# Kernel tuning notes

Hardware: AMD Instinct MI355X
Metric: run time of the kernel (lower is better)

## Reference

```python
import jax, jax.numpy as jnp
import numpy as np
import itertools

# ---- static configuration (matches init_kwargs) ----
LS = [0, 1, 2, 3]            # spherical harmonic degrees, parity (-1)^l
MUL = 128                    # channel multiplicity of hklm / output
N_EDGES = 16384
DIMS = [2 * l + 1 for l in LS]
Y_DIM = sum(DIMS)                        # 16
H_DIM = sum(d * MUL for d in DIMS)       # 2048
Y_OFF = np.cumsum([0] + DIMS).tolist()
H_OFF = np.cumsum([0] + [d * MUL for d in DIMS]).tolist()

# ---- real-basis O(3) Clebsch-Gordan coefficients (numpy, setup-time) ----
def _su2_generators(l):
    m = np.arange(-l, l + 1)
    Lz = np.diag(m).astype(np.complex128)
    vals = np.sqrt(l * (l + 1) - m[:-1] * (m[:-1] + 1))
    Lp = np.zeros((2 * l + 1, 2 * l + 1), np.complex128)
    Lp[np.arange(1, 2 * l + 1), np.arange(2 * l)] = vals
    Lm = Lp.T.copy()
    return (Lp + Lm) / 2.0, (Lp - Lm) / 2.0j, Lz

def _c2r(l):
    # unitary change of basis: complex SH -> real SH
    d = 2 * l + 1
    U = np.zeros((d, d), np.complex128)
    U[l, l] = 1.0
    s2 = 1.0 / np.sqrt(2.0)
    for m in range(1, l + 1):
        U[l + m, l + m] = (-1) ** m * s2
        U[l + m, l - m] = s2
        U[l - m, l + m] = -1j * (-1) ** m * s2
        U[l - m, l - m] = 1j * s2
    return U

def _real_generators(l):
    U = _c2r(l)
    return [np.real(-1j * (U @ L @ U.conj().T)) for L in _su2_generators(l)]

def _cg(l1, l2, l3):
    # invariant tensor = null space of the summed infinitesimal rotation action
    G1, G2, G3 = _real_generators(l1), _real_generators(l2), _real_generators(l3)
    d1, d2, d3 = 2 * l1 + 1, 2 * l2 + 1, 2 * l3 + 1
    I1, I2, I3 = np.eye(d1), np.eye(d2), np.eye(d3)
    rows = []
    for k in range(3):
        rows.append(np.kron(np.kron(G1[k], I2), I3)
                    + np.kron(np.kron(I1, G2[k]), I3)
                    + np.kron(np.kron(I1, I2), G3[k]))
    K = np.concatenate(rows, axis=0)
    _, s, Vt = np.linalg.svd(K)
    c = Vt[-1].reshape(d1, d2, d3)
    c = c / np.linalg.norm(c)
    c = c * np.sign(c.reshape(-1)[np.argmax(np.abs(c))])  # deterministic sign
    return c

PATHS = []
_CG_LIST = []
for (i1, l1), (i2, l2), (i3, l3) in itertools.product(enumerate(LS), enumerate(LS), enumerate(LS)):
    # triangle inequality + O3 parity selection rule ((-1)^l parities)
    if abs(l1 - l2) <= l3 <= l1 + l2 and (l1 + l2 + l3) % 2 == 0:
        PATHS.append((i1, i2, i3))
        _CG_LIST.append(_cg(l1, l2, l3))
N_PATHS = len(PATHS)                    # 23
W_DIM = N_PATHS * MUL                   # 2944
CG_OFF = np.cumsum([0] + [c.size for c in _CG_LIST]).tolist()
CGC_NP = np.concatenate([c.reshape(-1) for c in _CG_LIST]).astype(np.float32)


def setup_inputs() -> dict:
    key = jax.random.key(0)
    k1, k2, k3 = jax.random.split(key, 3)
    return {
        "Ylm": jax.random.normal(k1, (N_EDGES, Y_DIM), jnp.float32),
        "hklm": jax.random.normal(k2, (N_EDGES, H_DIM), jnp.float32),
        "weight": jax.random.normal(k3, (N_EDGES, W_DIM), jnp.float32),
        "CGC": jnp.asarray(CGC_NP),   # registered buffer in the torch module
    }


def reference(Ylm, hklm, weight, CGC):
    # segmented tensor product 'abcu,a,bu,cu' with per-path weight fused in:
    # out[n, c, u] += sum_{a,b} CG_p[a,b,c] * w_p[n,u] * Y[n,a] * h[n,b,u]
    N = Ylm.shape[0]
    out = jnp.zeros((N, H_DIM), Ylm.dtype)
    for p, (i1, i2, i3) in enumerate(PATHS):
        d1, d2, d3 = DIMS[i1], DIMS[i2], DIMS[i3]
        cg = CGC[CG_OFF[p]:CG_OFF[p + 1]].reshape(d1, d2, d3)
        y = Ylm[:, Y_OFF[i1]:Y_OFF[i1] + d1]
        h = hklm[:, H_OFF[i2]:H_OFF[i2] + d2 * MUL].reshape(N, d2, MUL)
        w = weight[:, p * MUL:(p + 1) * MUL]
        z = jnp.einsum('abc,na,nbu->ncu', cg, y, h) * w[:, None, :]
        out = out.at[:, H_OFF[i3]:H_OFF[i3] + d3 * MUL].add(z.reshape(N, d3 * MUL))
    return out
```

## Files before the change

kernel.cpp:

```cpp
#include <hip/hip_runtime.h>


#define BS 256
#define EPB 2
#define TPE 128
#define YD 16
#define HD 2048
#define WD 2944
#define NROW 99

typedef float f4 __attribute__((ext_vector_type(4)));

#define FOR_PATHS(X) \
  X(0, 0,0,0,    0,  0) \
  X(1, 0,1,1,    1,  1) \
  X(2, 0,2,2,   10,  4) \
  X(3, 0,3,3,   35,  9) \
  X(4, 1,0,1,   84, 16) \
  X(5, 1,1,0,   93, 19) \
  X(6, 1,1,2,  102, 20) \
  X(7, 1,2,1,  147, 25) \
  X(8, 1,2,3,  192, 28) \
  X(9, 1,3,2,  297, 35) \
  X(10,2,0,2,  402, 40) \
  X(11,2,1,1,  427, 45) \
  X(12,2,1,3,  472, 48) \
  X(13,2,2,0,  577, 55) \
  X(14,2,2,2,  602, 56) \
  X(15,2,3,1,  727, 61) \
  X(16,2,3,3,  832, 64) \
  X(17,3,0,3, 1077, 71) \
  X(18,3,1,2, 1126, 78) \
  X(19,3,2,1, 1231, 83) \
  X(20,3,2,3, 1336, 86) \
  X(21,3,3,0, 1581, 93) \
  X(22,3,3,2, 1630, 94)

__host__ __device__ constexpr int coff(int l) {
  return l == 0 ? 0 : (l == 1 ? 1 : (l == 2 ? 4 : 9));
}

__global__ __launch_bounds__(BS, 8) void etp_kernel(
    const float* __restrict__ Y, const float* __restrict__ H,
    const float* __restrict__ W, const float* __restrict__ CG,
    float* __restrict__ O) {
  const int g = threadIdx.x >> 7;
  const int u = threadIdx.x & 127;
  const size_t n = (size_t)blockIdx.x * EPB + g;

  __shared__ __align__(16) float Bsm[EPB][NROW * 8];
  __shared__ float ysm[EPB][YD];

  { const int t = threadIdx.x;
    if (t < EPB * YD) {
      const int e = t >> 4, c = t & 15;
      ysm[e][c] = Y[(size_t)(blockIdx.x * EPB + e) * YD + c];
    } }
  __syncthreads();

#define BUILD(P, L1, L2, L3, CGO, RO) { \
    constexpr int d1 = 2*(L1)+1, d2 = 2*(L2)+1, d3 = 2*(L3)+1; \
    if (u < d2 * d3) { \
      const int m3 = u / d2, m2 = u - m3 * d2; \
      float s = 0.f; \
      _Pragma("unroll") \
      for (int a = 0; a < d1; ++a) \
        s += CG[(CGO) + (a * d2 + m2) * d3 + m3] * ysm[g][coff(L1) + a]; \
      Bsm[g][((RO) + m3) * 8 + m2] = s; \
    } }
  FOR_PATHS(BUILD)
#undef BUILD
  __syncthreads();

  const float* __restrict__ Hn = H + n * HD + u;
  const float* __restrict__ Wn = W + n * WD + u;
  float* __restrict__ On = O + n * HD + u;

  float acc[YD];
#pragma unroll
  for (int c = 0; c < YD; ++c) acc[c] = 0.f;

#define DOP(P, L2, L3, RO) { \
    constexpr int d2 = 2*(L2)+1, d3 = 2*(L3)+1; \
    const float wv = Wn[(P) * TPE]; \
    _Pragma("unroll") \
    for (int m3 = 0; m3 < d3; ++m3) { \
      const f4* row = (const f4*)&Bsm[g][((RO) + m3) * 8]; \
      float br[8]; \
      *(f4*)&br[0] = row[0]; \
      if (d2 > 4) *(f4*)&br[4] = row[1]; \
      float s = 0.f; \
      _Pragma("unroll") \
      for (int m2 = 0; m2 < d2; ++m2) s += br[m2] * hh[m2]; \
      acc[coff(L3) + m3] += s * wv; \
    } }

  {
    float hh[1];
    hh[0] = Hn[(coff(0) + 0) * TPE];
    DOP(0, 0, 0, 0)  DOP(4, 0, 1, 16)  DOP(10, 0, 2, 40)  DOP(17, 0, 3, 71)
  }
  {
    float hh[3];
#pragma unroll
    for (int m = 0; m < 3; ++m) hh[m] = Hn[(coff(1) + m) * TPE];
    DOP(1, 1, 1, 1)  DOP(5, 1, 0, 19)  DOP(6, 1, 2, 20)
    DOP(11, 1, 1, 45)  DOP(12, 1, 3, 48)  DOP(18, 1, 2, 78)
  }
  {
    float hh[5];
#pragma unroll
    for (int m = 0; m < 5; ++m) hh[m] = Hn[(coff(2) + m) * TPE];
    DOP(2, 2, 2, 4)  DOP(7, 2, 1, 25)  DOP(8, 2, 3, 28)
    DOP(13, 2, 0, 55)  DOP(14, 2, 2, 56)  DOP(19, 2, 1, 83)  DOP(20, 2, 3, 86)
  }
  {
    float hh[7];
#pragma unroll
    for (int m = 0; m < 7; ++m) hh[m] = Hn[(coff(3) + m) * TPE];
    DOP(3, 3, 3, 9)  DOP(9, 3, 2, 35)  DOP(15, 3, 1, 61)
    DOP(16, 3, 3, 64)  DOP(21, 3, 0, 93)  DOP(22, 3, 2, 94)
  }
#undef DOP

#pragma unroll
  for (int c = 0; c < YD; ++c)
    __builtin_nontemporal_store(acc[c], &On[c * TPE]);
}

extern "C" void kernel_launch(void* const* d_in, const int* in_sizes, int n_in,
                              void* d_out, int out_size, void* d_ws, size_t ws_size,
                              hipStream_t stream) {
  const float* Y  = (const float*)d_in[0];
  const float* H  = (const float*)d_in[1];
  const float* W  = (const float*)d_in[2];
  const float* CG = (const float*)d_in[3];
  float* O = (float*)d_out;

  const int n_edges = in_sizes[0] / YD;
  etp_kernel<<<n_edges / EPB, BS, 0, stream>>>(Y, H, W, CG, O);
}
```

Baseline: 101.9 us.

## Process four channels per thread with float4 loads, eight edges per block

```diff
diff --git a/kernel.cpp b/kernel.cpp
--- a/kernel.cpp
+++ b/kernel.cpp
@@ -2,8 +2,8 @@
 
 
 #define BS 256
-#define EPB 2
-#define TPE 128
+#define GSZ 32
+#define EPB 8
 #define YD 16
 #define HD 2048
 #define WD 2944
@@ -40,12 +40,12 @@
   return l == 0 ? 0 : (l == 1 ? 1 : (l == 2 ? 4 : 9));
 }
 
-__global__ __launch_bounds__(BS, 8) void etp_kernel(
+__global__ __launch_bounds__(BS, 4) void etp_kernel(
     const float* __restrict__ Y, const float* __restrict__ H,
     const float* __restrict__ W, const float* __restrict__ CG,
     float* __restrict__ O) {
-  const int g = threadIdx.x >> 7;
-  const int u = threadIdx.x & 127;
+  const int g = threadIdx.x >> 5;
+  const int l = threadIdx.x & 31;
   const size_t n = (size_t)blockIdx.x * EPB + g;
 
   __shared__ __align__(16) float Bsm[EPB][NROW * 8];
@@ -60,64 +60,67 @@
 
 #define BUILD(P, L1, L2, L3, CGO, RO) { \
     constexpr int d1 = 2*(L1)+1, d2 = 2*(L2)+1, d3 = 2*(L3)+1; \
-    if (u < d2 * d3) { \
-      const int m3 = u / d2, m2 = u - m3 * d2; \
-      float s = 0.f; \
-      _Pragma("unroll") \
-      for (int a = 0; a < d1; ++a) \
-        s += CG[(CGO) + (a * d2 + m2) * d3 + m3] * ysm[g][coff(L1) + a]; \
-      Bsm[g][((RO) + m3) * 8 + m2] = s; \
-    } }
+    _Pragma("unroll") \
+    for (int it = 0; it < (d2 * d3 + GSZ - 1) / GSZ; ++it) { \
+      const int idx = l + it * GSZ; \
+      if (idx < d2 * d3) { \
+        const int m3 = idx / d2, m2 = idx - m3 * d2; \
+        float s = 0.f; \
+        _Pragma("unroll") \
+        for (int a = 0; a < d1; ++a) \
+          s += CG[(CGO) + (a * d2 + m2) * d3 + m3] * ysm[g][coff(L1) + a]; \
+        Bsm[g][((RO) + m3) * 8 + m2] = s; \
+      } } }
   FOR_PATHS(BUILD)
 #undef BUILD
   __syncthreads();
 
-  const float* __restrict__ Hn = H + n * HD + u;
-  const float* __restrict__ Wn = W + n * WD + u;
-  float* __restrict__ On = O + n * HD + u;
+  const f4* __restrict__ Hp = (const f4*)(H + n * HD);
+  const f4* __restrict__ Wp = (const f4*)(W + n * WD);
+  f4* __restrict__ Op = (f4*)(O + n * HD);
 
-  float acc[YD];
+  f4 acc[YD];
 #pragma unroll
-  for (int c = 0; c < YD; ++c) acc[c] = 0.f;
+  for (int c = 0; c < YD; ++c) acc[c] = (f4)0.f;
 
 #define DOP(P, L2, L3, RO) { \
     constexpr int d2 = 2*(L2)+1, d3 = 2*(L3)+1; \
-    const float wv = Wn[(P) * TPE]; \
+    const f4 wv = Wp[(P) * GSZ + l]; \
     _Pragma("unroll") \
     for (int m3 = 0; m3 < d3; ++m3) { \
       const f4* row = (const f4*)&Bsm[g][((RO) + m3) * 8]; \
       float br[8]; \
       *(f4*)&br[0] = row[0]; \
       if (d2 > 4) *(f4*)&br[4] = row[1]; \
-      float s = 0.f; \
+      f4 s = (f4)0.f; \
       _Pragma("unroll") \
       for (int m2 = 0; m2 < d2; ++m2) s += br[m2] * hh[m2]; \
       acc[coff(L3) + m3] += s * wv; \
     } }
 
   {
-    float hh[1];
-    hh[0] = Hn[(coff(0) + 0) * TPE];
+    f4 hh[1];
+    hh[0] = Hp[(coff(0) + 0) * GSZ + l];
     DOP(0, 0, 0, 0)  DOP(4, 0, 1, 16)  DOP(10, 0, 2, 40)  DOP(17, 0, 3, 71)
   }
   {
-    float hh[3];
+    f4 hh[3];
 #pragma unroll
-    for (int m = 0; m < 3; ++m) hh[m] = Hn[(coff(1) + m) * TPE];
+    for (int m = 0; m < 3; ++m) hh[m] = Hp[(coff(1) + m) * GSZ + l];
     DOP(1, 1, 1, 1)  DOP(5, 1, 0, 19)  DOP(6, 1, 2, 20)
     DOP(11, 1, 1, 45)  DOP(12, 1, 3, 48)  DOP(18, 1, 2, 78)
   }
   {
-    float hh[5];
+    f4 hh[5];
 #pragma unroll
-    for (int m = 0; m < 5; ++m) hh[m] = Hn[(coff(2) + m) * TPE];
+    for (int m = 0; m < 5; ++m) hh[m] = Hp[(coff(2) + m) * GSZ + l];
     DOP(2, 2, 2, 4)  DOP(7, 2, 1, 25)  DOP(8, 2, 3, 28)
     DOP(13, 2, 0, 55)  DOP(14, 2, 2, 56)  DOP(19, 2, 1, 83)  DOP(20, 2, 3, 86)
   }
   {
-    float hh[7];
+    f4 hh[7];
 #pragma unroll
-    for (int m = 0; m < 7; ++m) hh[m] = Hn[(coff(3) + m) * TPE];
+    for (int m = 0; m < 7; ++m) hh[m] = Hp[(coff(3) + m) * GSZ + l];
     DOP(3, 3, 3, 9)  DOP(9, 3, 2, 35)  DOP(15, 3, 1, 61)
     DOP(16, 3, 3, 64)  DOP(21, 3, 0, 93)  DOP(22, 3, 2, 94)
   }
@@ -125,7 +128,7 @@
 
 #pragma unroll
   for (int c = 0; c < YD; ++c)
-    __builtin_nontemporal_store(acc[c], &On[c * TPE]);
+    __builtin_nontemporal_store(acc[c], &Op[c * GSZ + l]);
 }
 
 extern "C" void kernel_launch(void* const* d_in, const int* in_sizes, int n_in,
```

Result: slower. 108.0 us (+6.0%).
